# Optimization experiments

Measured on AMD Instinct MI355X. Metric: run time of the kernel, lower is better.

## Reference

```python
import jax, jax.numpy as jnp
import numpy as np

E, F, H = 8, 5632, 2048
T = 8192


def setup_inputs() -> dict:
    key = jax.random.key(0)
    k1, k2, k3, k4 = jax.random.split(key, 4)
    s_w = 1.0 / np.sqrt(H)
    return {
        "expert_idx": 3,
        "hidden_states": jax.random.normal(k1, (T, H), dtype=jnp.float32),
        "fc1_1": jax.random.normal(k2, (E, F, H), dtype=jnp.float32) * s_w,
        "fc1_2": jax.random.normal(k3, (E, F, H), dtype=jnp.float32) * s_w,
        "fc2": jax.random.normal(k4, (E, H, F), dtype=jnp.float32) * (1.0 / np.sqrt(F)),
    }


def reference(expert_idx, hidden_states, fc1_1, fc1_2, fc2):
    # Select this expert's weights: [F,H], [F,H], [H,F]
    w1 = fc1_1[expert_idx]
    w2 = fc1_2[expert_idx]
    w3 = fc2[expert_idx]
    # SwiGLU FFN: silu(x @ w1^T) * (x @ w2^T) @ w3^T
    gate = jnp.einsum("th,fh->tf", hidden_states, w1)
    up = jnp.einsum("th,fh->tf", hidden_states, w2)
    fc1_out = jax.nn.silu(gate) * up  # [T, F]
    out = jnp.einsum("tf,hf->th", fc1_out, w3)  # [T, H]
    return out
```

## Files before the change

### kernel.cpp

```cpp
#include <hip/hip_runtime.h>
#include <hip/hip_bf16.h>

#define T_DIM 8192
#define H_DIM 2048
#define F_DIM 5632

typedef __attribute__((ext_vector_type(4))) float f32x4;
typedef __attribute__((ext_vector_type(8))) short bf16x8;

static __device__ __forceinline__ void gload16(const void* g, void* l) {
    __builtin_amdgcn_global_load_lds(
        (const __attribute__((address_space(1))) void*)g,
        (__attribute__((address_space(3))) void*)l,
        16, 0, 0);
}

static __device__ __forceinline__ unsigned short f2bf(float f) {
    unsigned int u = __float_as_uint(f);
    u += 0x7fffu + ((u >> 16) & 1u);
    return (unsigned short)(u >> 16);
}

static __device__ __forceinline__ float bf2f(unsigned short u) {
    return __uint_as_float(((unsigned int)u) << 16);
}

__global__ __launch_bounds__(256)
void cvt_x(const float* __restrict__ src, unsigned short* __restrict__ dst, long n)
{
    const long stride = (long)gridDim.x * blockDim.x;
    for (long i = (long)blockIdx.x * blockDim.x + threadIdx.x; i * 4 < n; i += stride) {
        const float4 v = *(const float4*)(src + i * 4);
        ushort4 o;
        o.x = f2bf(v.x); o.y = f2bf(v.y); o.z = f2bf(v.z); o.w = f2bf(v.w);
        *(ushort4*)(dst + i * 4) = o;
    }
}

__global__ __launch_bounds__(256)
void cvt_w(const float* __restrict__ w1, const float* __restrict__ w2,
           const float* __restrict__ w3, const int* __restrict__ eidx,
           unsigned short* __restrict__ W1b, unsigned short* __restrict__ W2b,
           unsigned short* __restrict__ W3b)
{
    const long seg = (long)F_DIM * H_DIM;
    const long e   = (long)(*eidx);
    const long nchunks = 3 * seg / 4;
    const long stride = (long)gridDim.x * blockDim.x;
    for (long i = (long)blockIdx.x * blockDim.x + threadIdx.x; i < nchunks; i += stride) {
        const long t = i * 4;
        const int  s = (int)(t / seg);
        const long o = t - (long)s * seg;
        const float* src = (s == 0 ? w1 : s == 1 ? w2 : w3) + e * seg + o;
        unsigned short* dst = (s == 0 ? W1b : s == 1 ? W2b : W3b) + o;
        const float4 v = *(const float4*)src;
        ushort4 ov;
        ov.x = f2bf(v.x); ov.y = f2bf(v.y); ov.z = f2bf(v.z); ov.w = f2bf(v.w);
        *(ushort4*)dst = ov;
    }
}

static __device__ __forceinline__ void stage_half(const unsigned short* __restrict__ g,
                                                  long grow0, long ldk, long kb,
                                                  unsigned short* l, int t, int i0)
{
    const int r  = t >> 3;
    const int cc = ((t & 7) ^ (r & 7)) << 3;
    #pragma unroll
    for (int i = i0; i < i0 + 2; ++i)
        gload16(g + (grow0 + i * 64 + r) * ldk + kb + cc,
                l + i * 4096 + t * 8);
}

static __device__ __forceinline__ bf16x8 ldsfrag(const unsigned short* base,
                                                 int row, int kk, int q)
{
    return *(const bf16x8*)(base + row * 64 + (((kk * 4 + q) ^ (row & 7)) << 3));
}

#define PHASE_BODY(p, STAGE_STMT)                                              \
    {                                                                          \
        bf16x8 af[2][2];                                                       \
        _Pragma("unroll")                                                      \
        for (int l_ = 0; l_ < 2; ++l_)                                         \
            _Pragma("unroll")                                                  \
            for (int kk = 0; kk < 2; ++kk)                                     \
                af[l_][kk] = ldsfrag(la, wm * 128 + (p) * 32 + l_ * 16 + lr, kk, q); \
        STAGE_STMT;                                                            \
        __builtin_amdgcn_s_barrier();                                          \
        __builtin_amdgcn_s_setprio(1);                                         \
        _Pragma("unroll")                                                      \
        for (int l_ = 0; l_ < 2; ++l_)                                         \
            _Pragma("unroll")                                                  \
            for (int ni = 0; ni < 4; ++ni)                                     \
                _Pragma("unroll")                                              \
                for (int kk = 0; kk < 2; ++kk)                                 \
                    acc[(p) * 2 + l_][ni] = __builtin_amdgcn_mfma_f32_16x16x32_bf16( \
                        af[l_][kk], bf[ni][kk], acc[(p) * 2 + l_][ni], 0, 0, 0);     \
        __builtin_amdgcn_s_setprio(0);                                         \
        __builtin_amdgcn_s_barrier();                                          \
    }

template<int MODE, int KDIM, int NBN>
__global__ __launch_bounds__(512, 2)
void gemm256(const unsigned short* __restrict__ A,
             const unsigned short* __restrict__ B,
             void* outp, unsigned short* gate)
{
    constexpr int  NK   = KDIM / 64;
    constexpr long NTOT = (long)NBN * 256;

    __shared__ __align__(16) unsigned short sAll[4 * 16384];

    const int tid  = threadIdx.x;
    const int lane = tid & 63;
    const int wid  = tid >> 6;
    const int wm   = wid >> 2;
    const int wn   = wid & 3;
    const int q    = lane >> 4;
    const int lr   = lane & 15;

    const int nwg = gridDim.x;
    const int bid = blockIdx.x;
    const int cpx = nwg >> 3;
    const int swz = (bid & 7) * cpx + (bid >> 3);
    const int bm  = swz / NBN;
    const int bn  = swz % NBN;

    const long arow0 = (long)bm * 256;
    const long brow0 = (long)bn * 256;
    const long tileBase = ((long)bm * NBN + bn) * 65536L;

    f32x4 acc[8][4] = {};

    stage_half(A, arow0, KDIM, 0,  sAll,          tid, 0);
    stage_half(A, arow0, KDIM, 0,  sAll,          tid, 2);
    stage_half(B, brow0, KDIM, 0,  sAll + 16384,  tid, 0);
    stage_half(B, brow0, KDIM, 0,  sAll + 16384,  tid, 2);
    stage_half(B, brow0, KDIM, 64, sAll + 49152,  tid, 0);
    stage_half(B, brow0, KDIM, 64, sAll + 49152,  tid, 2);

    for (int j = 0; j < NK - 1; ++j) {
        unsigned short* la = sAll + (j & 1) * 32768;
        unsigned short* lb = la + 16384;
        unsigned short* na = sAll + ((j + 1) & 1) * 32768;
        stage_half(A, arow0, KDIM, (long)(j + 1) * 64, na, tid, 0);
        stage_half(A, arow0, KDIM, (long)(j + 1) * 64, na, tid, 2);
        asm volatile("s_waitcnt vmcnt(8)" ::: "memory");
        __builtin_amdgcn_s_barrier();

        bf16x8 bf[4][2];
        #pragma unroll
        for (int ni = 0; ni < 4; ++ni)
            #pragma unroll
            for (int kk = 0; kk < 2; ++kk)
                bf[ni][kk] = ldsfrag(lb, wn * 64 + ni * 16 + lr, kk, q);

        PHASE_BODY(0, {})
        PHASE_BODY(1, { if (j + 2 < NK) stage_half(B, brow0, KDIM, (long)(j + 2) * 64, lb, tid, 0); })
        PHASE_BODY(2, { if (j + 2 < NK) stage_half(B, brow0, KDIM, (long)(j + 2) * 64, lb, tid, 2); })
        PHASE_BODY(3, {})
    }

    ushort4 pre[32];
    {
        const int j = NK - 1;
        unsigned short* la = sAll + (j & 1) * 32768;
        unsigned short* lb = la + 16384;
        asm volatile("s_waitcnt vmcnt(0)" ::: "memory");
        __builtin_amdgcn_s_barrier();

        if constexpr (MODE == 4) {
            #pragma unroll
            for (int mi = 0; mi < 8; ++mi)
                #pragma unroll
                for (int ni = 0; ni < 4; ++ni)
                    pre[mi * 4 + ni] = *(const ushort4*)(
                        gate + tileBase + (long)(mi * 4 + ni) * 2048 + (long)tid * 4);
        }

        bf16x8 bf[4][2];
        #pragma unroll
        for (int ni = 0; ni < 4; ++ni)
            #pragma unroll
            for (int kk = 0; kk < 2; ++kk)
                bf[ni][kk] = ldsfrag(lb, wn * 64 + ni * 16 + lr, kk, q);

        PHASE_BODY(0, {})
        PHASE_BODY(1, {})
        PHASE_BODY(2, {})
        PHASE_BODY(3, {})
    }

    if constexpr (MODE == 3) {
        #pragma unroll
        for (int mi = 0; mi < 8; ++mi)
            #pragma unroll
            for (int ni = 0; ni < 4; ++ni) {
                ushort4 o;
                o.x = f2bf(acc[mi][ni][0]); o.y = f2bf(acc[mi][ni][1]);
                o.z = f2bf(acc[mi][ni][2]); o.w = f2bf(acc[mi][ni][3]);
                *(ushort4*)(gate + tileBase + (long)(mi * 4 + ni) * 2048 + (long)tid * 4) = o;
            }
    } else {
        const long orow = (long)bm * 256 + wm * 128;
        const long ocol = (long)bn * 256 + wn * 64;
        #pragma unroll
        for (int mi = 0; mi < 8; ++mi)
            #pragma unroll
            for (int ni = 0; ni < 4; ++ni)
                #pragma unroll
                for (int r = 0; r < 4; ++r) {
                    const long idx = (orow + mi * 16 + q * 4 + r) * NTOT + (ocol + ni * 16 + lr);
                    if constexpr (MODE == 0) {
                        ((float*)outp)[idx] = acc[mi][ni][r];
                    } else if constexpr (MODE == 1) {
                        ((unsigned short*)outp)[idx] = f2bf(acc[mi][ni][r]);
                    } else if constexpr (MODE == 2) {
                        const float g = bf2f(gate[idx]);
                        const float h = __fdividef(g, 1.0f + __expf(-g)) * acc[mi][ni][r];
                        ((unsigned short*)outp)[idx] = f2bf(h);
                    } else {
                        const float g = bf2f((&pre[mi * 4 + ni].x)[r]);
                        const float h = __fdividef(g, 1.0f + __expf(-g)) * acc[mi][ni][r];
                        ((unsigned short*)outp)[idx] = f2bf(h);
                    }
                }
    }
}

extern "C" void kernel_launch(void* const* d_in, const int* in_sizes, int n_in,
                              void* d_out, int out_size, void* d_ws, size_t ws_size,
                              hipStream_t stream)
{
    const int*   eidx = (const int*)d_in[0];
    const float* x    = (const float*)d_in[1];
    const float* w1   = (const float*)d_in[2];
    const float* w2   = (const float*)d_in[3];
    const float* w3   = (const float*)d_in[4];
    float* out = (float*)d_out;

    const size_t SZ_X = (size_t)T_DIM * H_DIM;
    const size_t SZ_W = (size_t)F_DIM * H_DIM;
    const size_t SZ_H = (size_t)T_DIM * F_DIM;

    unsigned short* Xb  = (unsigned short*)d_ws;
    unsigned short* W1b = Xb  + SZ_X;
    unsigned short* W2b = W1b + SZ_W;
    unsigned short* W3b = W2b + SZ_W;
    unsigned short* Hb  = W3b + SZ_W;
    unsigned short* Gb  = Hb  + SZ_H;

    const size_t need_blocked = (SZ_X + 3 * SZ_W + 2 * SZ_H) * 2;

    cvt_x<<<2048, 256, 0, stream>>>(x, Xb, (long)SZ_X);
    cvt_w<<<2048, 256, 0, stream>>>(w1, w2, w3, eidx, W1b, W2b, W3b);

    constexpr int NBN1 = F_DIM / 256;
    constexpr int NBN2 = H_DIM / 256;
    const int grid1 = (T_DIM / 256) * NBN1;
    const int grid2 = (T_DIM / 256) * NBN2;

    if (ws_size >= need_blocked) {
        gemm256<3, H_DIM, NBN1><<<grid1, 512, 0, stream>>>(Xb, W1b, nullptr, Gb);
        gemm256<4, H_DIM, NBN1><<<grid1, 512, 0, stream>>>(Xb, W2b, Hb, Gb);
    } else {
        gemm256<1, H_DIM, NBN1><<<grid1, 512, 0, stream>>>(Xb, W1b, Hb, nullptr);
        gemm256<2, H_DIM, NBN1><<<grid1, 512, 0, stream>>>(Xb, W2b, Hb, Hb);
    }
    gemm256<0, F_DIM, NBN2><<<grid2, 512, 0, stream>>>(Hb, W3b, out, nullptr);
}
```

Before: 599.4 us.

## Fuse gate and up GEMMs into persistent kernel with per-block tile schedule

Replaces the two separate fc1 GEMM launches with one persistent kernel of 256 blocks. Each block walks 2 or 3 output tiles, computing the gate tile first, applying SiLU and parking it in a per-block bf16 slot, then computing the up tile and writing the product straight to H. The staging pipeline now runs continuously across tile boundaries, which removes a launch and the separate 704-block tail. It also changes the fc2 GEMM to a fixed 256-block grid with a simplified loop. The uneven 3-vs-2 tile split across blocks can cause load imbalance, and the round trip of the gate tile through global memory remains.

```diff
diff --git a/kernel.cpp b/kernel.cpp
--- a/kernel.cpp
+++ b/kernel.cpp
@@ -101,15 +101,28 @@
         __builtin_amdgcn_s_barrier();                                          \
     }
 
-template<int MODE, int KDIM, int NBN>
+struct StageP { const unsigned short* B; long arow, brow, kb; };
+static __device__ __forceinline__ StageP decode_f(int f, int t0p,
+    const unsigned short* W1, const unsigned short* W2)
+{
+    const int vt = f >> 5, j = f & 31, rt = vt >> 1;
+    const int tp = t0p + rt * 32;
+    const int bm = tp / 22, bn = tp - bm * 22;
+    StageP s;
+    s.B    = (vt & 1) ? W2 : W1;
+    s.arow = (long)bm * 256;
+    s.brow = (long)bn * 256;
+    s.kb   = (long)j * 64;
+    return s;
+}
+
 __global__ __launch_bounds__(512, 2)
-void gemm256(const unsigned short* __restrict__ A,
-             const unsigned short* __restrict__ B,
-             void* outp, unsigned short* gate)
-{
-    constexpr int  NK   = KDIM / 64;
-    constexpr long NTOT = (long)NBN * 256;
-
+void gemm_fc1(const unsigned short* __restrict__ X,
+              const unsigned short* __restrict__ W1,
+              const unsigned short* __restrict__ W2,
+              unsigned short* __restrict__ Hout,
+              unsigned short* Gb)
+{
     __shared__ __align__(16) unsigned short sAll[4 * 16384];
 
     const int tid  = threadIdx.x;
@@ -120,6 +133,116 @@
     const int q    = lane >> 4;
     const int lr   = lane & 15;
 
+    const int bid  = blockIdx.x;
+    const int t0p  = (bid & 7) * 88 + (bid >> 3);
+    const int ntt  = (bid < 192) ? 3 : 2;
+    const int FTOT = ntt * 64;
+
+    unsigned short* Gslot = Gb + (long)bid * 65536;
+
+    f32x4 acc[8][4] = {};
+
+    {
+        StageP s0 = decode_f(0, t0p, W1, W2);
+        stage_half(X,    s0.arow, H_DIM, 0, sAll,         tid, 0);
+        stage_half(X,    s0.arow, H_DIM, 0, sAll,         tid, 2);
+        stage_half(s0.B, s0.brow, H_DIM, 0, sAll + 16384, tid, 0);
+        stage_half(s0.B, s0.brow, H_DIM, 0, sAll + 16384, tid, 2);
+        StageP s1 = decode_f(1, t0p, W1, W2);
+        stage_half(s1.B, s1.brow, H_DIM, s1.kb, sAll + 49152, tid, 0);
+        stage_half(s1.B, s1.brow, H_DIM, s1.kb, sAll + 49152, tid, 2);
+    }
+
+    for (int f = 0; f < FTOT; ++f) {
+        unsigned short* la = sAll + (f & 1) * 32768;
+        unsigned short* lb = la + 16384;
+
+        if (f + 1 < FTOT) {
+            StageP sn = decode_f(f + 1, t0p, W1, W2);
+            unsigned short* na = sAll + ((f + 1) & 1) * 32768;
+            stage_half(X, sn.arow, H_DIM, sn.kb, na, tid, 0);
+            stage_half(X, sn.arow, H_DIM, sn.kb, na, tid, 2);
+            asm volatile("s_waitcnt vmcnt(8)" ::: "memory");
+        } else {
+            asm volatile("s_waitcnt vmcnt(0)" ::: "memory");
+        }
+        __builtin_amdgcn_s_barrier();
+
+        bf16x8 bf[4][2];
+        #pragma unroll
+        for (int ni = 0; ni < 4; ++ni)
+            #pragma unroll
+            for (int kk = 0; kk < 2; ++kk)
+                bf[ni][kk] = ldsfrag(lb, wn * 64 + ni * 16 + lr, kk, q);
+
+        PHASE_BODY(0, {})
+        PHASE_BODY(1, { if (f + 2 < FTOT) { StageP s2 = decode_f(f + 2, t0p, W1, W2);
+                                            stage_half(s2.B, s2.brow, H_DIM, s2.kb, lb, tid, 0); } })
+        PHASE_BODY(2, { if (f + 2 < FTOT) { StageP s2 = decode_f(f + 2, t0p, W1, W2);
+                                            stage_half(s2.B, s2.brow, H_DIM, s2.kb, lb, tid, 2); } })
+        PHASE_BODY(3, {})
+
+        const int fm = f & 63;
+        if (fm == 31) {
+            #pragma unroll
+            for (int mi = 0; mi < 8; ++mi)
+                #pragma unroll
+                for (int ni = 0; ni < 4; ++ni) {
+                    ushort4 o;
+                    #pragma unroll
+                    for (int r = 0; r < 4; ++r) {
+                        const float g = acc[mi][ni][r];
+                        const float s = __fdividef(g, 1.0f + __expf(-g));
+                        (&o.x)[r] = f2bf(s);
+                    }
+                    *(ushort4*)(Gslot + (mi * 4 + ni) * 2048 + tid * 4) = o;
+                    acc[mi][ni] = (f32x4){0.f, 0.f, 0.f, 0.f};
+                }
+        } else if (fm == 63) {
+            const int rt = f >> 6;
+            const int tp = t0p + rt * 32;
+            const int bm = tp / 22, bn = tp - bm * 22;
+            const long orow = (long)bm * 256 + wm * 128;
+            const long ocol = (long)bn * 256 + wn * 64;
+            #pragma unroll
+            for (int mi = 0; mi < 8; ++mi) {
+                ushort4 sg[4];
+                #pragma unroll
+                for (int ni = 0; ni < 4; ++ni)
+                    sg[ni] = *(const ushort4*)(Gslot + (mi * 4 + ni) * 2048 + tid * 4);
+                #pragma unroll
+                for (int ni = 0; ni < 4; ++ni) {
+                    #pragma unroll
+                    for (int r = 0; r < 4; ++r) {
+                        const float h = bf2f((&sg[ni].x)[r]) * acc[mi][ni][r];
+                        Hout[(orow + mi * 16 + q * 4 + r) * (long)F_DIM +
+                             (ocol + ni * 16 + lr)] = f2bf(h);
+                    }
+                    acc[mi][ni] = (f32x4){0.f, 0.f, 0.f, 0.f};
+                }
+            }
+        }
+    }
+}
+
+__global__ __launch_bounds__(512, 2)
+void gemm_out(const unsigned short* __restrict__ A,
+              const unsigned short* __restrict__ B,
+              float* __restrict__ Out)
+{
+    constexpr int NK  = F_DIM / 64;
+    constexpr int NBN = H_DIM / 256;
+
+    __shared__ __align__(16) unsigned short sAll[4 * 16384];
+
+    const int tid  = threadIdx.x;
+    const int lane = tid & 63;
+    const int wid  = tid >> 6;
+    const int wm   = wid >> 2;
+    const int wn   = wid & 3;
+    const int q    = lane >> 4;
+    const int lr   = lane & 15;
+
     const int nwg = gridDim.x;
     const int bid = blockIdx.x;
     const int cpx = nwg >> 3;
@@ -129,24 +252,28 @@
 
     const long arow0 = (long)bm * 256;
     const long brow0 = (long)bn * 256;
-    const long tileBase = ((long)bm * NBN + bn) * 65536L;
 
     f32x4 acc[8][4] = {};
 
-    stage_half(A, arow0, KDIM, 0,  sAll,          tid, 0);
-    stage_half(A, arow0, KDIM, 0,  sAll,          tid, 2);
-    stage_half(B, brow0, KDIM, 0,  sAll + 16384,  tid, 0);
-    stage_half(B, brow0, KDIM, 0,  sAll + 16384,  tid, 2);
-    stage_half(B, brow0, KDIM, 64, sAll + 49152,  tid, 0);
-    stage_half(B, brow0, KDIM, 64, sAll + 49152,  tid, 2);
-
-    for (int j = 0; j < NK - 1; ++j) {
+    stage_half(A, arow0, F_DIM, 0,  sAll,          tid, 0);
+    stage_half(A, arow0, F_DIM, 0,  sAll,          tid, 2);
+    stage_half(B, brow0, F_DIM, 0,  sAll + 16384,  tid, 0);
+    stage_half(B, brow0, F_DIM, 0,  sAll + 16384,  tid, 2);
+    stage_half(B, brow0, F_DIM, 64, sAll + 49152,  tid, 0);
+    stage_half(B, brow0, F_DIM, 64, sAll + 49152,  tid, 2);
+
+    for (int j = 0; j < NK; ++j) {
         unsigned short* la = sAll + (j & 1) * 32768;
         unsigned short* lb = la + 16384;
-        unsigned short* na = sAll + ((j + 1) & 1) * 32768;
-        stage_half(A, arow0, KDIM, (long)(j + 1) * 64, na, tid, 0);
-        stage_half(A, arow0, KDIM, (long)(j + 1) * 64, na, tid, 2);
-        asm volatile("s_waitcnt vmcnt(8)" ::: "memory");
+
+        if (j + 1 < NK) {
+            unsigned short* na = sAll + ((j + 1) & 1) * 32768;
+            stage_half(A, arow0, F_DIM, (long)(j + 1) * 64, na, tid, 0);
+            stage_half(A, arow0, F_DIM, (long)(j + 1) * 64, na, tid, 2);
+            asm volatile("s_waitcnt vmcnt(8)" ::: "memory");
+        } else {
+            asm volatile("s_waitcnt vmcnt(0)" ::: "memory");
+        }
         __builtin_amdgcn_s_barrier();
 
         bf16x8 bf[4][2];
@@ -157,76 +284,21 @@
                 bf[ni][kk] = ldsfrag(lb, wn * 64 + ni * 16 + lr, kk, q);
 
         PHASE_BODY(0, {})
-        PHASE_BODY(1, { if (j + 2 < NK) stage_half(B, brow0, KDIM, (long)(j + 2) * 64, lb, tid, 0); })
-        PHASE_BODY(2, { if (j + 2 < NK) stage_half(B, brow0, KDIM, (long)(j + 2) * 64, lb, tid, 2); })
+        PHASE_BODY(1, { if (j + 2 < NK) stage_half(B, brow0, F_DIM, (long)(j + 2) * 64, lb, tid, 0); })
+        PHASE_BODY(2, { if (j + 2 < NK) stage_half(B, brow0, F_DIM, (long)(j + 2) * 64, lb, tid, 2); })
         PHASE_BODY(3, {})
     }
 
-    ushort4 pre[32];
-    {
-        const int j = NK - 1;
-        unsigned short* la = sAll + (j & 1) * 32768;
-        unsigned short* lb = la + 16384;
-        asm volatile("s_waitcnt vmcnt(0)" ::: "memory");
-        __builtin_amdgcn_s_barrier();
-
-        if constexpr (MODE == 4) {
-            #pragma unroll
-            for (int mi = 0; mi < 8; ++mi)
-                #pragma unroll
-                for (int ni = 0; ni < 4; ++ni)
-                    pre[mi * 4 + ni] = *(const ushort4*)(
-                        gate + tileBase + (long)(mi * 4 + ni) * 2048 + (long)tid * 4);
-        }
-
-        bf16x8 bf[4][2];
+    const long orow = (long)bm * 256 + wm * 128;
+    const long ocol = (long)bn * 256 + wn * 64;
+    #pragma unroll
+    for (int mi = 0; mi < 8; ++mi)
         #pragma unroll
         for (int ni = 0; ni < 4; ++ni)
             #pragma unroll
-            for (int kk = 0; kk < 2; ++kk)
-                bf[ni][kk] = ldsfrag(lb, wn * 64 + ni * 16 + lr, kk, q);
-
-        PHASE_BODY(0, {})
-        PHASE_BODY(1, {})
-        PHASE_BODY(2, {})
-        PHASE_BODY(3, {})
-    }
-
-    if constexpr (MODE == 3) {
-        #pragma unroll
-        for (int mi = 0; mi < 8; ++mi)
-            #pragma unroll
-            for (int ni = 0; ni < 4; ++ni) {
-                ushort4 o;
-                o.x = f2bf(acc[mi][ni][0]); o.y = f2bf(acc[mi][ni][1]);
-                o.z = f2bf(acc[mi][ni][2]); o.w = f2bf(acc[mi][ni][3]);
-                *(ushort4*)(gate + tileBase + (long)(mi * 4 + ni) * 2048 + (long)tid * 4) = o;
-            }
-    } else {
-        const long orow = (long)bm * 256 + wm * 128;
-        const long ocol = (long)bn * 256 + wn * 64;
-        #pragma unroll
-        for (int mi = 0; mi < 8; ++mi)
-            #pragma unroll
-            for (int ni = 0; ni < 4; ++ni)
-                #pragma unroll
-                for (int r = 0; r < 4; ++r) {
-                    const long idx = (orow + mi * 16 + q * 4 + r) * NTOT + (ocol + ni * 16 + lr);
-                    if constexpr (MODE == 0) {
-                        ((float*)outp)[idx] = acc[mi][ni][r];
-                    } else if constexpr (MODE == 1) {
-                        ((unsigned short*)outp)[idx] = f2bf(acc[mi][ni][r]);
-                    } else if constexpr (MODE == 2) {
-                        const float g = bf2f(gate[idx]);
-                        const float h = __fdividef(g, 1.0f + __expf(-g)) * acc[mi][ni][r];
-                        ((unsigned short*)outp)[idx] = f2bf(h);
-                    } else {
-                        const float g = bf2f((&pre[mi * 4 + ni].x)[r]);
-                        const float h = __fdividef(g, 1.0f + __expf(-g)) * acc[mi][ni][r];
-                        ((unsigned short*)outp)[idx] = f2bf(h);
-                    }
-                }
-    }
+            for (int r = 0; r < 4; ++r)
+                Out[(orow + mi * 16 + q * 4 + r) * (long)H_DIM + (ocol + ni * 16 + lr)]
+                    = acc[mi][ni][r];
 }
 
 extern "C" void kernel_launch(void* const* d_in, const int* in_sizes, int n_in,
@@ -251,22 +323,9 @@
     unsigned short* Hb  = W3b + SZ_W;
     unsigned short* Gb  = Hb  + SZ_H;
 
-    const size_t need_blocked = (SZ_X + 3 * SZ_W + 2 * SZ_H) * 2;
-
     cvt_x<<<2048, 256, 0, stream>>>(x, Xb, (long)SZ_X);
     cvt_w<<<2048, 256, 0, stream>>>(w1, w2, w3, eidx, W1b, W2b, W3b);
 
-    constexpr int NBN1 = F_DIM / 256;
-    constexpr int NBN2 = H_DIM / 256;
-    const int grid1 = (T_DIM / 256) * NBN1;
-    const int grid2 = (T_DIM / 256) * NBN2;
-
-    if (ws_size >= need_blocked) {
-        gemm256<3, H_DIM, NBN1><<<grid1, 512, 0, stream>>>(Xb, W1b, nullptr, Gb);
-        gemm256<4, H_DIM, NBN1><<<grid1, 512, 0, stream>>>(Xb, W2b, Hb, Gb);
-    } else {
-        gemm256<1, H_DIM, NBN1><<<grid1, 512, 0, stream>>>(Xb, W1b, Hb, nullptr);
-        gemm256<2, H_DIM, NBN1><<<grid1, 512, 0, stream>>>(Xb, W2b, Hb, Hb);
-    }
-    gemm256<0, F_DIM, NBN2><<<grid2, 512, 0, stream>>>(Hb, W3b, out, nullptr);
-}
+    gemm_fc1<<<256, 512, 0, stream>>>(Xb, W1b, W2b, Hb, Gb);
+    gemm_out<<<256, 512, 0, stream>>>(Hb, W3b, out);
+}
```

Result: slower. 950.6 us (+58.6%).
